# Kernel tuning notes

Measured on AMD Instinct MI355X. Metric: run time of the kernel, lower is better.

The kernel has to match this reference:

```python
import jax, jax.numpy as jnp
import numpy as np

PAD_TOKEN_ID = 0
EPS = 1e-12  # torch F.normalize eps

B_Q, L_Q = 64, 32
B_D, L_D = 512, 256
HID, OUT = 768, 128
VOCAB = 30522


def setup_inputs() -> dict:
    key = jax.random.key(0)
    k1, k2, k3, k4, k5 = jax.random.split(key, 5)
    return {
        "q_hidden": jax.random.normal(k1, (B_Q, L_Q, HID), dtype=jnp.float32),
        "d_hidden": jax.random.normal(k2, (B_D, L_D, HID), dtype=jnp.float32),
        "d_input_ids": jax.random.randint(k3, (B_D, L_D), 0, VOCAB, dtype=jnp.int32),
        "skiplist": jax.random.randint(k4, (64,), 0, VOCAB, dtype=jnp.int32),
        "W": jax.random.normal(k5, (OUT, HID), dtype=jnp.float32) * (HID ** -0.5),
    }


def _l2norm(x):
    n = jnp.sqrt(jnp.sum(x * x, axis=-1, keepdims=True))
    return x / jnp.maximum(n, EPS)


def reference(q_hidden, d_hidden, d_input_ids, skiplist, W):
    # query(): linear proj + L2 normalize      (B_q, L_q, F)
    Q = _l2norm(jnp.einsum("blh,fh->blf", q_hidden, W))
    # doc(): linear proj + L2 normalize + mask (B_d, L_d, F)
    D = _l2norm(jnp.einsum("blh,fh->blf", d_hidden, W))
    is_pad = d_input_ids == PAD_TOKEN_ID
    is_punct = jnp.any(d_input_ids[..., None] == skiplist, axis=-1)
    d_mask = (~is_pad) & (~is_punct)                     # (B_d, L_d)
    D = D * d_mask[..., None].astype(D.dtype)
    # forward(): reshape to (B, N, L, F) with B = min(B_q, B_d)
    B = min(q_hidden.shape[0], d_hidden.shape[0])
    Qr = Q.reshape(B, -1, L_Q, OUT)                      # (B, 1, L_q, F)
    Dr = D.reshape(B, -1, L_D, OUT)                      # (B, N_p, L_d, F)
    Mr = d_mask.reshape(B, -1, L_D)                      # (B, N_p, L_d)
    # similarity(): cosine MaxSim, Q @ D^T with broadcast over N_p
    sim = jnp.einsum("bqf,bndf->bnqd", Qr[:, 0], Dr)     # (B, N_p, L_q, L_d)
    sim = jnp.where(Mr[:, :, None, :], sim, -jnp.inf)
    sms = jnp.max(sim, axis=-1).mean(axis=-1)            # (B, N_p)
    return sms
```

## Files before the change

### kernel.cpp

```cpp
#include <hip/hip_runtime.h>
#include <stdint.h>

typedef float  f32x4 __attribute__((ext_vector_type(4)));
typedef short  s16x8 __attribute__((ext_vector_type(8)));
typedef unsigned int u32;
typedef unsigned short u16;
typedef unsigned int u32x4 __attribute__((ext_vector_type(4)));

#define HID 768
#define OUTF 128
#define LQ 32
#define LD 256

__device__ __forceinline__ u32 pk_rna(float lo, float hi) {
    u32 a = __builtin_bit_cast(u32, lo) + 0x8000u;
    u32 b = __builtin_bit_cast(u32, hi) + 0x8000u;
    return __builtin_amdgcn_perm(b, a, 0x07060302u);
}
__device__ __forceinline__ u16 f2bf(float x) {
    return (u16)((__builtin_bit_cast(u32, x) + 0x8000u) >> 16);
}
__device__ __forceinline__ s16x8 cvt8(f32x4 lo, f32x4 hi) {
    union { u32 u[4]; s16x8 v; } ua;
    ua.u[0] = pk_rna(lo[0], lo[1]);
    ua.u[1] = pk_rna(lo[2], lo[3]);
    ua.u[2] = pk_rna(hi[0], hi[1]);
    ua.u[3] = pk_rna(hi[2], hi[3]);
    return ua.v;
}

__global__ __launch_bounds__(256) void wconv(const float* __restrict__ W,
                                             u32* __restrict__ Wb3d) {
    int t = blockIdx.x * 256 + threadIdx.x;
    int j2   = t & 3;
    int lane = (t >> 2) & 63;
    int cf   = (t >> 8) & 7;
    int kk   = t >> 11;
    int l15 = lane & 15, g4 = lane >> 4;
    int f = cf * 16 + l15;
    int k = kk * 32 + g4 * 8 + j2 * 2;
    const float* src = W + (size_t)f * HID + k;
    Wb3d[t] = pk_rna(src[0], src[1]);
}

__global__ __launch_bounds__(256) void qproj(const float* __restrict__ qh,
                                             const u16* __restrict__ Wb3,
                                             u16* __restrict__ Qb) {
    const int b = blockIdx.x;
    const int tid = threadIdx.x;
    const int w = tid >> 6, lane = tid & 63, g = lane >> 4, l15 = lane & 15;

    f32x4 acc[2][2] = {};
    const float* A0 = qh + ((size_t)b * LQ + l15) * HID + g * 8;
    const float* A1 = A0 + 16 * HID;
    const u16* Bp = Wb3 + w * 1024 + lane * 8;

    for (int kk = 0; kk < 24; ++kk) {
        f32x4 x0 = *(const f32x4*)A0;
        f32x4 x1 = *(const f32x4*)(A0 + 4);
        f32x4 y0 = *(const f32x4*)A1;
        f32x4 y1 = *(const f32x4*)(A1 + 4);
        s16x8 b0 = *(const s16x8*)(Bp);
        s16x8 b1 = *(const s16x8*)(Bp + 512);
        s16x8 a0 = cvt8(x0, x1);
        s16x8 a1 = cvt8(y0, y1);
        acc[0][0] = __builtin_amdgcn_mfma_f32_16x16x32_bf16(a0, b0, acc[0][0], 0, 0, 0);
        acc[0][1] = __builtin_amdgcn_mfma_f32_16x16x32_bf16(a0, b1, acc[0][1], 0, 0, 0);
        acc[1][0] = __builtin_amdgcn_mfma_f32_16x16x32_bf16(a1, b0, acc[1][0], 0, 0, 0);
        acc[1][1] = __builtin_amdgcn_mfma_f32_16x16x32_bf16(a1, b1, acc[1][1], 0, 0, 0);
        A0 += 32; A1 += 32; Bp += 4096;
    }

    __shared__ float part[4][32];
    __shared__ float invl[32];
#pragma unroll
    for (int rf = 0; rf < 2; ++rf)
#pragma unroll
        for (int reg = 0; reg < 4; ++reg) {
            float ss = acc[rf][0][reg] * acc[rf][0][reg] + acc[rf][1][reg] * acc[rf][1][reg];
            ss += __shfl_xor(ss, 1); ss += __shfl_xor(ss, 2);
            ss += __shfl_xor(ss, 4); ss += __shfl_xor(ss, 8);
            if (l15 == 0) part[w][rf * 16 + g * 4 + reg] = ss;
        }
    __syncthreads();
    if (tid < 32) {
        float ss = part[0][tid] + part[1][tid] + part[2][tid] + part[3][tid];
        invl[tid] = 1.f / fmaxf(sqrtf(ss), 1e-12f);
    }
    __syncthreads();
#pragma unroll
    for (int rf = 0; rf < 2; ++rf)
#pragma unroll
        for (int cf = 0; cf < 2; ++cf)
#pragma unroll
            for (int reg = 0; reg < 4; ++reg) {
                int q = rf * 16 + g * 4 + reg;
                int f = w * 32 + cf * 16 + l15;
                Qb[(size_t)b * LQ * OUTF + q * OUTF + f] = f2bf(acc[rf][cf][reg] * invl[q]);
            }
}

__global__ __launch_bounds__(512, 2) void dmax(const float* __restrict__ dh,
                                               const int* __restrict__ ids,
                                               const int* __restrict__ skiplist,
                                               const u16* __restrict__ Wb3,
                                               const u16* __restrict__ Qb,
                                               float* __restrict__ out) {
    const int bid = blockIdx.x;
    const int tid = threadIdx.x;
    const int w = tid >> 6, lane = tid & 63, g4 = lane >> 4, l15 = lane & 15;
    const int qh_ = w >> 2;

    __shared__ __align__(16) u16 stg[2][12288];
    __shared__ __align__(16) u16 outb[2][2048];
    __shared__ __align__(16) float nrm[2][16][8];
    __shared__ float red[8][16];
    __shared__ int ms[512];
    __shared__ int sk[64];

#define PADOF(v) (((v) / 192) * 1536 + (((((v) % 192)) * 8) ^ ((((v) / 192) & 7) << 4)))
    const int pad0 = PADOF(2 * tid), pad1 = PADOF(2 * tid + 1024), pad2 = PADOF(2 * tid + 2048);

    const int swz = (l15 & 7) << 4, sw45 = swz & 48, sw6 = swz & 64;
    const int aoffE = l15 * 1536 + ((g4 * 16) ^ sw45) + sw6;
    const int aoffO = l15 * 1536 + ((g4 * 16) ^ sw45) + 64 - sw6;
    const int doffE = l15 * 256 + ((g4 * 16) ^ sw45) + sw6;
    const int doffO = l15 * 256 + ((g4 * 16) ^ sw45) + 64 - sw6;

    f32x4 LA0, LA1, LA2, LA3, LA4, LA5;
    s16x8 Qr0, Qr1, Qr2, Qr3;
    float rmaxH[4] = {-INFINITY, -INFINITY, -INFINITY, -INFINITY};

#define SLABBASE(sab) ((const char*)dh + (size_t)(bid + (((sab) >> 4) << 8)) * 786432 \
                       + (size_t)((sab) & 15) * 49152)

#define LISSUE(sab) { const char* gb_ = SLABBASE(sab) + 32 * tid; \
    LA0 = *(const f32x4*)(gb_);          LA1 = *(const f32x4*)(gb_ + 16); \
    LA2 = *(const f32x4*)(gb_ + 16384);  LA3 = *(const f32x4*)(gb_ + 16400); \
    LA4 = *(const f32x4*)(gb_ + 32768);  LA5 = *(const f32x4*)(gb_ + 32784); }

#define WSTORE(P) { char* sb_ = (char*)&stg[P][0]; u32x4 q_; \
    q_[0] = pk_rna(LA0[0], LA0[1]); q_[1] = pk_rna(LA0[2], LA0[3]); \
    q_[2] = pk_rna(LA1[0], LA1[1]); q_[3] = pk_rna(LA1[2], LA1[3]); \
    *(u32x4*)(sb_ + pad0) = q_; \
    q_[0] = pk_rna(LA2[0], LA2[1]); q_[1] = pk_rna(LA2[2], LA2[3]); \
    q_[2] = pk_rna(LA3[0], LA3[1]); q_[3] = pk_rna(LA3[2], LA3[3]); \
    *(u32x4*)(sb_ + pad1) = q_; \
    q_[0] = pk_rna(LA4[0], LA4[1]); q_[1] = pk_rna(LA4[2], LA4[3]); \
    q_[2] = pk_rna(LA5[0], LA5[1]); q_[3] = pk_rna(LA5[2], LA5[3]); \
    *(u32x4*)(sb_ + pad2) = q_; }

#define QLOAD(doc_) { const u16* qp_ = Qb + (size_t)((bid + (doc_) * 256) >> 3) * 4096 \
                      + (qh_ * 16 + l15) * 128 + g4 * 8; \
    Qr0 = *(const s16x8*)(qp_);      Qr1 = *(const s16x8*)(qp_ + 32); \
    Qr2 = *(const s16x8*)(qp_ + 64); Qr3 = *(const s16x8*)(qp_ + 96); }

#define GEMMN(P, s_) { \
    const char* Ab_ = (const char*)&stg[P][0]; \
    u16* ob_ = &outb[(s_) & 1][0]; \
    f32x4 ac0_ = {}, ac1_ = {}; \
    _Pragma("unroll") for (int kkp = 0; kkp < 12; ++kkp) { \
        s16x8 ae_ = *(const s16x8*)(Ab_ + aoffE + kkp * 128); \
        s16x8 ao_ = *(const s16x8*)(Ab_ + aoffO + kkp * 128); \
        ac0_ = __builtin_amdgcn_mfma_f32_16x16x32_bf16(ae_, Bf[2 * kkp],     ac0_, 0, 0, 0); \
        ac1_ = __builtin_amdgcn_mfma_f32_16x16x32_bf16(ao_, Bf[2 * kkp + 1], ac1_, 0, 0, 0); \
    } \
    f32x4 aG_ = ac0_ + ac1_; \
    _Pragma("unroll") for (int rg = 0; rg < 4; ++rg) { \
        float ss_ = aG_[rg] * aG_[rg]; \
        ss_ += __shfl_xor(ss_, 1); ss_ += __shfl_xor(ss_, 2); \
        ss_ += __shfl_xor(ss_, 4); ss_ += __shfl_xor(ss_, 8); \
        if (l15 == 0) nrm[(s_) & 1][g4 * 4 + rg][w] = ss_; \
        int dr_ = g4 * 4 + rg; \
        int of_ = (dr_ * 256 + (w * 16 + l15) * 2) ^ ((dr_ & 7) << 4); \
        *(u16*)((char*)ob_ + of_) = f2bf(aG_[rg]); \
    } }

#define TAIL(sb) { \
    if ((w & 3) == ((sb) & 3)) { \
        const char* Db_ = (const char*)&outb[(sb) & 1][0]; \
        s16x8 d0_ = *(const s16x8*)(Db_ + doffE); \
        s16x8 d1_ = *(const s16x8*)(Db_ + doffO); \
        s16x8 d2_ = *(const s16x8*)(Db_ + doffE + 128); \
        s16x8 d3_ = *(const s16x8*)(Db_ + doffO + 128); \
        f32x4 s2_ = {}; \
        s2_ = __builtin_amdgcn_mfma_f32_16x16x32_bf16(Qr0, d0_, s2_, 0, 0, 0); \
        s2_ = __builtin_amdgcn_mfma_f32_16x16x32_bf16(Qr1, d1_, s2_, 0, 0, 0); \
        s2_ = __builtin_amdgcn_mfma_f32_16x16x32_bf16(Qr2, d2_, s2_, 0, 0, 0); \
        s2_ = __builtin_amdgcn_mfma_f32_16x16x32_bf16(Qr3, d3_, s2_, 0, 0, 0); \
        f32x4 n0_ = *(const f32x4*)&nrm[(sb) & 1][l15][0]; \
        f32x4 n1_ = *(const f32x4*)&nrm[(sb) & 1][l15][4]; \
        float ssv_ = (n0_[0] + n0_[1] + n0_[2] + n0_[3]) \
                   + (n1_[0] + n1_[1] + n1_[2] + n1_[3]); \
        float inv_ = 1.f / fmaxf(sqrtf(ssv_), 1e-12f); \
        int keep_ = ms[(((sb) >> 4) << 8) + (((sb) & 15) << 4) + l15]; \
        _Pragma("unroll") for (int rg = 0; rg < 4; ++rg) { \
            float v_ = keep_ ? s2_[rg] * inv_ : -INFINITY; \
            rmaxH[rg] = fmaxf(rmaxH[rg], v_); } \
    } \
    if (((sb) & 15) == 15) { \
        _Pragma("unroll") for (int rg = 0; rg < 4; ++rg) { \
            float v_ = rmaxH[rg]; \
            v_ = fmaxf(v_, __shfl_xor(v_, 1)); v_ = fmaxf(v_, __shfl_xor(v_, 2)); \
            v_ = fmaxf(v_, __shfl_xor(v_, 4)); v_ = fmaxf(v_, __shfl_xor(v_, 8)); \
            if (l15 == 0) red[w][g4 * 4 + rg] = v_; \
            rmaxH[rg] = -INFINITY; } \
        asm volatile("s_waitcnt lgkmcnt(0)" ::: "memory"); \
        __builtin_amdgcn_s_barrier(); \
        if (tid < 32) { \
            int qi_ = tid & 15; \
            int base_ = (tid < 16) ? 0 : 4; \
            float m_ = fmaxf(fmaxf(red[base_][qi_], red[base_ + 1][qi_]), \
                             fmaxf(red[base_ + 2][qi_], red[base_ + 3][qi_])); \
            m_ += __shfl_xor(m_, 1); m_ += __shfl_xor(m_, 2); \
            m_ += __shfl_xor(m_, 4); m_ += __shfl_xor(m_, 8); \
            m_ += __shfl_xor(m_, 16); \
            if (tid == 0) out[bid + (((sb) >> 4) << 8)] = m_ * (1.f / 32.f); } \
        if ((sb) == 15) { QLOAD(1); } \
    } }

#define SLABSTEP(s_, PG_) { \
    GEMMN(PG_, s_); \
    __builtin_amdgcn_sched_barrier(0); \
    if ((s_) + 1 < 32) WSTORE(((s_) + 1) & 1); \
    __builtin_amdgcn_sched_barrier(0); \
    if ((s_) + 2 < 32) LISSUE((s_) + 2); \
    asm volatile("s_waitcnt lgkmcnt(0)" ::: "memory"); \
    __builtin_amdgcn_s_barrier(); \
    TAIL(s_); }

    LISSUE(0);

    s16x8 Bf[24];
#pragma unroll
    for (int kk = 0; kk < 24; ++kk)
        Bf[kk] = *(const s16x8*)(Wb3 + (size_t)(kk * 8 + w) * 512 + lane * 8);

    if (tid < 64) sk[tid] = skiplist[tid];
    asm volatile("s_waitcnt lgkmcnt(0)" ::: "memory");
    __builtin_amdgcn_s_barrier();
    {
        int d_ = tid >> 8, r_ = tid & 255;
        int id_ = ids[(size_t)(bid + d_ * 256) * 256 + r_];
        int keep_ = (id_ != 0);
#pragma unroll
        for (int j = 0; j < 64; ++j) keep_ &= (id_ != sk[j]);
        ms[tid] = keep_;
    }
    WSTORE(0);
    LISSUE(1);
    QLOAD(0);
    asm volatile("s_waitcnt lgkmcnt(0)" ::: "memory");
    __builtin_amdgcn_s_barrier();

    for (int j = 0; j < 16; ++j) {
        SLABSTEP(2 * j, 0);
        SLABSTEP(2 * j + 1, 1);
    }
}

extern "C" void kernel_launch(void* const* d_in, const int* in_sizes, int n_in,
                              void* d_out, int out_size, void* d_ws, size_t ws_size,
                              hipStream_t stream) {
    const float* q_hidden = (const float*)d_in[0];
    const float* d_hidden = (const float*)d_in[1];
    const int*   d_ids    = (const int*)d_in[2];
    const int*   skiplist = (const int*)d_in[3];
    const float* W        = (const float*)d_in[4];
    float* out = (float*)d_out;

    u16* Wb3 = (u16*)d_ws;
    u16* Qb  = (u16*)((char*)d_ws + 256 * 1024);

    wconv<<<192, 256, 0, stream>>>(W, (u32*)Wb3);
    qproj<<<64, 256, 0, stream>>>(q_hidden, Wb3, Qb);
    dmax<<<256, 512, 0, stream>>>(d_hidden, d_ids, skiplist, Wb3, Qb, out);
}
```

Measured before the change: 100.4 us.

## Split projection K dimension across two wave halves with 1024-thread blocks

Doubles the dmax block to 1024 threads. The two halves of the waves each compute half of the 768-deep projection, and the upper half passes its partial accumulators through a new shared buffer. The lower half then normalises the rows, and the MaxSim tail is deferred by one slab so it runs after the combine. This halves per-wave loads, bf16 conversion work and B-fragment registers, raising latency hiding. In exchange it adds shared memory traffic and an extra serial dependency on the partial-sum exchange.

```diff
diff --git a/kernel.cpp b/kernel.cpp
--- a/kernel.cpp
+++ b/kernel.cpp
@@ -5,7 +5,7 @@
 typedef short  s16x8 __attribute__((ext_vector_type(8)));
 typedef unsigned int u32;
 typedef unsigned short u16;
-typedef unsigned int u32x4 __attribute__((ext_vector_type(4)));
+typedef unsigned int u32x2 __attribute__((ext_vector_type(2)));
 
 #define HID 768
 #define OUTF 128
@@ -100,55 +100,55 @@
             }
 }
 
-__global__ __launch_bounds__(512, 2) void dmax(const float* __restrict__ dh,
-                                               const int* __restrict__ ids,
-                                               const int* __restrict__ skiplist,
-                                               const u16* __restrict__ Wb3,
-                                               const u16* __restrict__ Qb,
-                                               float* __restrict__ out) {
+__global__ __launch_bounds__(1024, 4) void dmax(const float* __restrict__ dh,
+                                                const int* __restrict__ ids,
+                                                const int* __restrict__ skiplist,
+                                                const u16* __restrict__ Wb3,
+                                                const u16* __restrict__ Qb,
+                                                float* __restrict__ out) {
     const int bid = blockIdx.x;
     const int tid = threadIdx.x;
     const int w = tid >> 6, lane = tid & 63, g4 = lane >> 4, l15 = lane & 15;
-    const int qh_ = w >> 2;
+    const int c = w & 7, h = w >> 3;
+    const int qh_ = h;
 
     __shared__ __align__(16) u16 stg[2][12288];
     __shared__ __align__(16) u16 outb[2][2048];
+    __shared__ __align__(16) float accx[2][8][64][4];
     __shared__ __align__(16) float nrm[2][16][8];
-    __shared__ float red[8][16];
+    __shared__ float red[16][16];
     __shared__ int ms[512];
     __shared__ int sk[64];
 
 #define PADOF(v) (((v) / 192) * 1536 + (((((v) % 192)) * 8) ^ ((((v) / 192) & 7) << 4)))
-    const int pad0 = PADOF(2 * tid), pad1 = PADOF(2 * tid + 1024), pad2 = PADOF(2 * tid + 2048);
+    const int pad0 = PADOF(tid), pad1 = PADOF(tid + 1024), pad2 = PADOF(tid + 2048);
 
     const int swz = (l15 & 7) << 4, sw45 = swz & 48, sw6 = swz & 64;
-    const int aoffE = l15 * 1536 + ((g4 * 16) ^ sw45) + sw6;
-    const int aoffO = l15 * 1536 + ((g4 * 16) ^ sw45) + 64 - sw6;
+    const int aoffEh = l15 * 1536 + ((g4 * 16) ^ sw45) + sw6 + h * 768;
+    const int aoffOh = l15 * 1536 + ((g4 * 16) ^ sw45) + 64 - sw6 + h * 768;
     const int doffE = l15 * 256 + ((g4 * 16) ^ sw45) + sw6;
     const int doffO = l15 * 256 + ((g4 * 16) ^ sw45) + 64 - sw6;
 
-    f32x4 LA0, LA1, LA2, LA3, LA4, LA5;
+    f32x4 LA0, LA1, LA2;
+    f32x4 accS;
     s16x8 Qr0, Qr1, Qr2, Qr3;
     float rmaxH[4] = {-INFINITY, -INFINITY, -INFINITY, -INFINITY};
 
 #define SLABBASE(sab) ((const char*)dh + (size_t)(bid + (((sab) >> 4) << 8)) * 786432 \
                        + (size_t)((sab) & 15) * 49152)
 
-#define LISSUE(sab) { const char* gb_ = SLABBASE(sab) + 32 * tid; \
-    LA0 = *(const f32x4*)(gb_);          LA1 = *(const f32x4*)(gb_ + 16); \
-    LA2 = *(const f32x4*)(gb_ + 16384);  LA3 = *(const f32x4*)(gb_ + 16400); \
-    LA4 = *(const f32x4*)(gb_ + 32768);  LA5 = *(const f32x4*)(gb_ + 32784); }
-
-#define WSTORE(P) { char* sb_ = (char*)&stg[P][0]; u32x4 q_; \
-    q_[0] = pk_rna(LA0[0], LA0[1]); q_[1] = pk_rna(LA0[2], LA0[3]); \
-    q_[2] = pk_rna(LA1[0], LA1[1]); q_[3] = pk_rna(LA1[2], LA1[3]); \
-    *(u32x4*)(sb_ + pad0) = q_; \
-    q_[0] = pk_rna(LA2[0], LA2[1]); q_[1] = pk_rna(LA2[2], LA2[3]); \
-    q_[2] = pk_rna(LA3[0], LA3[1]); q_[3] = pk_rna(LA3[2], LA3[3]); \
-    *(u32x4*)(sb_ + pad1) = q_; \
-    q_[0] = pk_rna(LA4[0], LA4[1]); q_[1] = pk_rna(LA4[2], LA4[3]); \
-    q_[2] = pk_rna(LA5[0], LA5[1]); q_[3] = pk_rna(LA5[2], LA5[3]); \
-    *(u32x4*)(sb_ + pad2) = q_; }
+#define LISSUE(sab) { const char* gb_ = SLABBASE(sab) + 16 * tid; \
+    LA0 = *(const f32x4*)(gb_); \
+    LA1 = *(const f32x4*)(gb_ + 16384); \
+    LA2 = *(const f32x4*)(gb_ + 32768); }
+
+#define WSTORE(P) { char* sb_ = (char*)&stg[P][0]; u32x2 d_; \
+    d_[0] = pk_rna(LA0[0], LA0[1]); d_[1] = pk_rna(LA0[2], LA0[3]); \
+    *(u32x2*)(sb_ + pad0) = d_; \
+    d_[0] = pk_rna(LA1[0], LA1[1]); d_[1] = pk_rna(LA1[2], LA1[3]); \
+    *(u32x2*)(sb_ + pad1) = d_; \
+    d_[0] = pk_rna(LA2[0], LA2[1]); d_[1] = pk_rna(LA2[2], LA2[3]); \
+    *(u32x2*)(sb_ + pad2) = d_; }
 
 #define QLOAD(doc_) { const u16* qp_ = Qb + (size_t)((bid + (doc_) * 256) >> 3) * 4096 \
                       + (qh_ * 16 + l15) * 128 + g4 * 8; \
@@ -157,27 +157,32 @@
 
 #define GEMMN(P, s_) { \
     const char* Ab_ = (const char*)&stg[P][0]; \
-    u16* ob_ = &outb[(s_) & 1][0]; \
     f32x4 ac0_ = {}, ac1_ = {}; \
-    _Pragma("unroll") for (int kkp = 0; kkp < 12; ++kkp) { \
-        s16x8 ae_ = *(const s16x8*)(Ab_ + aoffE + kkp * 128); \
-        s16x8 ao_ = *(const s16x8*)(Ab_ + aoffO + kkp * 128); \
+    _Pragma("unroll") for (int kkp = 0; kkp < 6; ++kkp) { \
+        s16x8 ae_ = *(const s16x8*)(Ab_ + aoffEh + kkp * 128); \
+        s16x8 ao_ = *(const s16x8*)(Ab_ + aoffOh + kkp * 128); \
         ac0_ = __builtin_amdgcn_mfma_f32_16x16x32_bf16(ae_, Bf[2 * kkp],     ac0_, 0, 0, 0); \
         ac1_ = __builtin_amdgcn_mfma_f32_16x16x32_bf16(ao_, Bf[2 * kkp + 1], ac1_, 0, 0, 0); \
     } \
-    f32x4 aG_ = ac0_ + ac1_; \
+    accS = ac0_ + ac1_; \
+    if (h) *(f32x4*)&accx[(s_) & 1][c][lane][0] = accS; }
+
+#define FINISH(s_) { if (!h) { \
+    f32x4 po_ = *(const f32x4*)&accx[(s_) & 1][c][lane][0]; \
+    f32x4 at_ = accS + po_; \
+    u16* ob_ = &outb[(s_) & 1][0]; \
     _Pragma("unroll") for (int rg = 0; rg < 4; ++rg) { \
-        float ss_ = aG_[rg] * aG_[rg]; \
+        float ss_ = at_[rg] * at_[rg]; \
         ss_ += __shfl_xor(ss_, 1); ss_ += __shfl_xor(ss_, 2); \
         ss_ += __shfl_xor(ss_, 4); ss_ += __shfl_xor(ss_, 8); \
-        if (l15 == 0) nrm[(s_) & 1][g4 * 4 + rg][w] = ss_; \
+        if (l15 == 0) nrm[(s_) & 1][g4 * 4 + rg][c] = ss_; \
         int dr_ = g4 * 4 + rg; \
-        int of_ = (dr_ * 256 + (w * 16 + l15) * 2) ^ ((dr_ & 7) << 4); \
-        *(u16*)((char*)ob_ + of_) = f2bf(aG_[rg]); \
-    } }
+        int of_ = (dr_ * 256 + (c * 16 + l15) * 2) ^ ((dr_ & 7) << 4); \
+        *(u16*)((char*)ob_ + of_) = f2bf(at_[rg]); \
+    } } }
 
 #define TAIL(sb) { \
-    if ((w & 3) == ((sb) & 3)) { \
+    if ((w & 7) == ((sb) & 7)) { \
         const char* Db_ = (const char*)&outb[(sb) & 1][0]; \
         s16x8 d0_ = *(const s16x8*)(Db_ + doffE); \
         s16x8 d1_ = *(const s16x8*)(Db_ + doffO); \
@@ -208,10 +213,10 @@
         asm volatile("s_waitcnt lgkmcnt(0)" ::: "memory"); \
         __builtin_amdgcn_s_barrier(); \
         if (tid < 32) { \
-            int qi_ = tid & 15; \
-            int base_ = (tid < 16) ? 0 : 4; \
-            float m_ = fmaxf(fmaxf(red[base_][qi_], red[base_ + 1][qi_]), \
-                             fmaxf(red[base_ + 2][qi_], red[base_ + 3][qi_])); \
+            int qh2_ = tid >> 4, qi_ = tid & 15; \
+            float m_ = red[qh2_ * 8][qi_]; \
+            _Pragma("unroll") for (int jj = 1; jj < 8; ++jj) \
+                m_ = fmaxf(m_, red[qh2_ * 8 + jj][qi_]); \
             m_ += __shfl_xor(m_, 1); m_ += __shfl_xor(m_, 2); \
             m_ += __shfl_xor(m_, 4); m_ += __shfl_xor(m_, 8); \
             m_ += __shfl_xor(m_, 16); \
@@ -227,19 +232,20 @@
     if ((s_) + 2 < 32) LISSUE((s_) + 2); \
     asm volatile("s_waitcnt lgkmcnt(0)" ::: "memory"); \
     __builtin_amdgcn_s_barrier(); \
-    TAIL(s_); }
+    FINISH(s_); \
+    if ((s_) > 0) TAIL((s_) - 1); }
 
     LISSUE(0);
 
-    s16x8 Bf[24];
-#pragma unroll
-    for (int kk = 0; kk < 24; ++kk)
-        Bf[kk] = *(const s16x8*)(Wb3 + (size_t)(kk * 8 + w) * 512 + lane * 8);
+    s16x8 Bf[12];
+#pragma unroll
+    for (int kk = 0; kk < 12; ++kk)
+        Bf[kk] = *(const s16x8*)(Wb3 + (size_t)((h * 12 + kk) * 8 + c) * 512 + lane * 8);
 
     if (tid < 64) sk[tid] = skiplist[tid];
     asm volatile("s_waitcnt lgkmcnt(0)" ::: "memory");
     __builtin_amdgcn_s_barrier();
-    {
+    if (tid < 512) {
         int d_ = tid >> 8, r_ = tid & 255;
         int id_ = ids[(size_t)(bid + d_ * 256) * 256 + r_];
         int keep_ = (id_ != 0);
@@ -257,6 +263,10 @@
         SLABSTEP(2 * j, 0);
         SLABSTEP(2 * j + 1, 1);
     }
+
+    asm volatile("s_waitcnt lgkmcnt(0)" ::: "memory");
+    __builtin_amdgcn_s_barrier();
+    TAIL(31);
 }
 
 extern "C" void kernel_launch(void* const* d_in, const int* in_sizes, int n_in,
@@ -274,5 +284,5 @@
 
     wconv<<<192, 256, 0, stream>>>(W, (u32*)Wb3);
     qproj<<<64, 256, 0, stream>>>(q_hidden, Wb3, Qb);
-    dmax<<<256, 512, 0, stream>>>(d_hidden, d_ids, skiplist, Wb3, Qb, out);
-}
+    dmax<<<256, 1024, 0, stream>>>(d_hidden, d_ids, skiplist, Wb3, Qb, out);
+}
```

After: 131.4 us. 30.9% more time.
